# Kernel tuning notes

Hardware: AMD Instinct MI355X
Metric: run time of the kernel (lower is better)

## Reference

```python
import jax, jax.numpy as jnp
import numpy as np

B, NT, NP, C, A = 8, 100, 300, 92, 64
EPS = 1e-7  # keras backend epsilon


def _lsa(cost):
    """Hungarian algorithm (Jonker-Volgenant style), cost [n, m] with n <= m.
    Equivalent to scipy.optimize.linear_sum_assignment."""
    n, m = cost.shape
    if n == 0:
        return np.zeros(0, np.int64), np.zeros(0, np.int64)
    u = np.zeros(n + 1)
    v = np.zeros(m + 1)
    p = np.zeros(m + 1, np.int64)
    way = np.zeros(m + 1, np.int64)
    for i in range(1, n + 1):
        p[0] = i
        j0 = 0
        minv = np.full(m + 1, np.inf)
        used = np.zeros(m + 1, bool)
        while True:
            used[j0] = True
            i0 = p[j0]
            cur = cost[i0 - 1] - u[i0] - v[1:]
            better = (~used[1:]) & (cur < minv[1:])
            minv[1:] = np.where(better, cur, minv[1:])
            way[1:] = np.where(better, j0, way[1:])
            cand = np.where(used[1:], np.inf, minv[1:])
            j1 = int(np.argmin(cand)) + 1
            delta = cand[j1 - 1]
            u[p[used]] += delta
            v[used] -= delta
            minv[~used] -= delta
            j0 = j1
            if p[j0] == 0:
                break
        while j0 != 0:
            j1 = way[j0]
            p[j0] = p[j1]
            j0 = j1
    cols = np.nonzero(p[1:])[0]
    rows = p[1:][cols] - 1
    return rows, cols


def _hungarian_mask(cost, num_objects):
    # mirrors MatchingAssignment.scipy_linear_assignment_mask
    masks = np.zeros(cost.shape, dtype=np.float32)
    for i in range(cost.shape[0]):
        n = int(num_objects[i])
        r, c = _lsa(cost[i, :n, :])
        masks[i][r, c] = 1.0
    return masks


def _focal(y, p):
    # tfa SigmoidFocalCrossEntropy: alpha=0.25, gamma=2.0, probabilities in
    p = jnp.clip(p, EPS, 1.0 - EPS)
    ce = -(y * jnp.log(p) + (1.0 - y) * jnp.log(1.0 - p))
    p_t = y * p + (1.0 - y) * (1.0 - p)
    alpha_f = y * 0.25 + (1.0 - y) * 0.75
    return jnp.sum(alpha_f * (1.0 - p_t) ** 2 * ce, -1)


def _iou_giou(b1, b2):
    # boxes are [ymin, xmin, ymax, xmax] (tfa convention)
    ay1, ax1, ay2, ax2 = b1[..., 0], b1[..., 1], b1[..., 2], b1[..., 3]
    by1, bx1, by2, bx2 = b2[..., 0], b2[..., 1], b2[..., 2], b2[..., 3]
    area_a = jnp.maximum(ay2 - ay1, 0.0) * jnp.maximum(ax2 - ax1, 0.0)
    area_b = jnp.maximum(by2 - by1, 0.0) * jnp.maximum(bx2 - bx1, 0.0)
    inter = (jnp.maximum(jnp.minimum(ay2, by2) - jnp.maximum(ay1, by1), 0.0)
             * jnp.maximum(jnp.minimum(ax2, bx2) - jnp.maximum(ax1, bx1), 0.0))
    union = area_a + area_b - inter
    iou = jnp.where(union > 0, inter / jnp.where(union > 0, union, 1.0), 0.0)
    enc = (jnp.maximum(jnp.maximum(ay2, by2) - jnp.minimum(ay1, by1), 0.0)
           * jnp.maximum(jnp.maximum(ax2, bx2) - jnp.minimum(ax1, bx1), 0.0))
    giou = iou - jnp.where(enc > 0, (enc - union) / jnp.where(enc > 0, enc, 1.0), 0.0)
    return iou, giou


def _cost_arrays(category, attribute, bbox, cat_preds, attribute_preds, box_preds):
    # CostArray: true -> [B,Nt,1,D], pred -> [B,1,Np,D], broadcast -> [B,Nt,Np]
    t_cat = category[:, :, None, :]
    p_cat = cat_preds[:, None, :, :]
    cat_match = jnp.sum((1.0 - p_cat) * t_cat, -1)
    cat_cost = -jnp.sum(jnp.log(p_cat + 1e-5) * t_cat, -1)
    attr_cost = _focal(attribute[:, :, None, :], attribute_preds[:, None, :, :])
    b_t = bbox[:, :, None, :]
    b_p = box_preds[:, None, :, :]
    iou, giou = _iou_giou(b_t, b_p)
    box_cost = 2.0 * (1.0 - giou) + 5.0 * jnp.mean(jnp.abs(b_t - b_p), -1)
    iou_arr = 1.0 - iou  # tfa GIoULoss(mode='iou') returns 1 - iou
    return cat_match, cat_cost, attr_cost, box_cost, iou_arr


def setup_inputs():
    key = jax.random.key(0)
    ks = jax.random.split(key, 9)
    category = jax.nn.one_hot(jax.random.randint(ks[0], (B, NT), 0, C), C, dtype=jnp.float32)
    attribute = (jax.random.uniform(ks[1], (B, NT, A)) < 0.3).astype(jnp.float32)
    yx = jax.random.uniform(ks[2], (B, NT, 2), maxval=0.8)
    hw = jax.random.uniform(ks[3], (B, NT, 2), minval=0.05, maxval=0.2)
    bbox = jnp.concatenate([yx, yx + hw], -1)
    num_objects = jax.random.randint(ks[4], (B,), 1, NT + 1).astype(jnp.int32)
    cat_preds = jax.nn.softmax(jax.random.normal(ks[5], (B, NP, C)), -1)
    attribute_preds = jax.nn.sigmoid(jax.random.normal(ks[6], (B, NP, A)))
    yxp = jax.random.uniform(ks[7], (B, NP, 2), maxval=0.8)
    hwp = jax.random.uniform(ks[8], (B, NP, 2), minval=0.05, maxval=0.2)
    box_preds = jnp.concatenate([yxp, yxp + hwp], -1)
    return dict(category=category, attribute=attribute, bbox=bbox,
                num_objects=num_objects, cat_preds=cat_preds,
                attribute_preds=attribute_preds, box_preds=box_preds)


def reference(category, attribute, bbox, num_objects, cat_preds, attribute_preds, box_preds):
    cat_match, cat_cost_arr, attr_cost_arr, box_cost_arr, iou_arr = _cost_arrays(
        category, attribute, bbox, cat_preds, attribute_preds, box_preds)

    # bipartite matching on CPU (mirrors tf.numpy_function + scipy)
    match_cost = np.asarray(cat_match + box_cost_arr, np.float64)
    mask = jnp.asarray(_hungarian_mask(match_cost, np.asarray(num_objects)))

    total_num_obj = jnp.sum(num_objects).astype(jnp.float32)
    total_num_preds = float(B * NP)

    category_cost = jnp.sum(mask * cat_cost_arr) / total_num_obj
    attribute_cost = jnp.sum(mask * attr_cost_arr) / total_num_obj
    box_cost = jnp.sum(mask * box_cost_arr) / total_num_obj

    # exist loss: keras CategoricalCrossentropy on single-channel probs
    assigned = jnp.max(mask, axis=1)[..., None]  # [B, Np, 1]
    yp = 1.0 - cat_preds[..., 0:1]
    pn = jnp.clip(yp / jnp.sum(yp, -1, keepdims=True), EPS, 1.0 - EPS)
    exist_loss = jnp.sum(-jnp.sum(assigned * jnp.log(pn), -1)) / total_num_preds

    total_loss = category_cost + attribute_cost + box_cost + exist_loss

    masked_iou = mask * iou_arr
    iou_metric = jnp.sum(masked_iou) / total_num_obj
    num_correct_50 = jnp.sum(masked_iou >= 0.5).astype(jnp.float32)
    map_50_95 = jnp.stack([jnp.sum(masked_iou >= r / 100.0).astype(jnp.float32)
                           for r in range(50, 100, 5)]).sum()
    num_predicted = jnp.sum(cat_preds[:, 1, :] < 0.5).astype(jnp.float32)
    mAP50 = num_correct_50 / num_predicted
    map_50_95 = map_50_95 / (num_predicted * 10.0)

    losses = jnp.stack([total_loss, category_cost, attribute_cost, box_cost, exist_loss])
    metrics = jnp.stack([iou_metric, mAP50, map_50_95])
    return losses, metrics
```

## Files before the change

kernel.cpp:

```cpp
#include <hip/hip_runtime.h>
#include <math.h>

#define Bb 8
#define NTt 100
#define NPp 300
#define Cc 92
#define Aa 64


__device__ __forceinline__ void iou_giou_f(const float* bt, const float* bp,
                                           float& iou, float& giou) {
  float ay1 = bt[0], ax1 = bt[1], ay2 = bt[2], ax2 = bt[3];
  float by1 = bp[0], bx1 = bp[1], by2 = bp[2], bx2 = bp[3];
  float area_a = fmaxf(ay2 - ay1, 0.0f) * fmaxf(ax2 - ax1, 0.0f);
  float area_b = fmaxf(by2 - by1, 0.0f) * fmaxf(bx2 - bx1, 0.0f);
  float inter = fmaxf(fminf(ay2, by2) - fmaxf(ay1, by1), 0.0f) *
                fmaxf(fminf(ax2, bx2) - fmaxf(ax1, bx1), 0.0f);
  float un = area_a + area_b - inter;
  iou = (un > 0.0f) ? (inter / un) : 0.0f;
  float enc = fmaxf(fmaxf(ay2, by2) - fminf(ay1, by1), 0.0f) *
              fmaxf(fmaxf(ax2, bx2) - fminf(ax1, bx1), 0.0f);
  giou = iou - ((enc > 0.0f) ? ((enc - un) / enc) : 0.0f);
}

__device__ __forceinline__ float box_cost_f(const float* bt, const float* bp,
                                            float& iou_out) {
  float iou, giou;
  iou_giou_f(bt, bp, iou, giou);
  iou_out = iou;
  float l1 = (fabsf(bt[0] - bp[0]) + fabsf(bt[1] - bp[1]) +
              fabsf(bt[2] - bp[2]) + fabsf(bt[3] - bp[3])) * 0.25f;
  return 2.0f * (1.0f - giou) + 5.0f * l1;
}


template <int CTRL>
__device__ __forceinline__ void dpp_fmin64(double& val) {
  union DU { double d; int i[2]; };
  DU a; a.d = val;
  int lo = __builtin_amdgcn_update_dpp(a.i[0], a.i[0], CTRL, 0xF, 0xF, false);
  int hi = __builtin_amdgcn_update_dpp(a.i[1], a.i[1], CTRL, 0xF, 0xF, false);
  DU o; o.i[0] = lo; o.i[1] = hi;
  val = fmin(val, o.d);
}

__device__ __forceinline__ double wave_fmin64_bcast(double m01) {
  double mvred = m01;
  dpp_fmin64<0x111>(mvred);
  dpp_fmin64<0x112>(mvred);
  dpp_fmin64<0x114>(mvred);
  dpp_fmin64<0x118>(mvred);
  dpp_fmin64<0x142>(mvred);
  dpp_fmin64<0x143>(mvred);
  union DU { double d; int i[2]; };
  DU w; w.d = mvred;
  DU r;
  r.i[0] = __builtin_amdgcn_readlane(w.i[0], 63);
  r.i[1] = __builtin_amdgcn_readlane(w.i[1], 63);
  return r.d;
}

__device__ __forceinline__ double read_u_row(double u_lo, double u_hi, int i0u) {
  int ridx = i0u - 1;
  int src = ridx & 63;
  union DU { double d; int i[2]; };
  DU a, bb, r;
  a.d = u_lo; bb.d = u_hi;
  int lo0 = __builtin_amdgcn_readlane(a.i[0], src);
  int hi0 = __builtin_amdgcn_readlane(a.i[1], src);
  int lo1 = __builtin_amdgcn_readlane(bb.i[0], src);
  int hi1 = __builtin_amdgcn_readlane(bb.i[1], src);
  bool hih = (ridx >> 6) != 0;
  r.i[0] = hih ? lo1 : lo0;
  r.i[1] = hih ? hi1 : hi0;
  return r.d;
}

__device__ __forceinline__ int sel5(int s, int a0, int a1, int a2, int a3, int a4) {
  int r = a4;
  r = (s == 3) ? a3 : r;
  r = (s == 2) ? a2 : r;
  r = (s == 1) ? a1 : r;
  r = (s == 0) ? a0 : r;
  return r;
}


__global__ void __launch_bounds__(64) cost_kernel(
    const float* __restrict__ category, const float* __restrict__ bbox,
    const float* __restrict__ box_preds, const float* __restrict__ cat_preds,
    float* __restrict__ cost, int* __restrict__ cls) {
  int bt = blockIdx.x;
  int b = bt / NTt;
  int lane = threadIdx.x;

  const float* crow = category + (size_t)bt * Cc;
  float c0 = (lane < Cc) ? crow[lane] : 0.0f;
  float c1 = (lane < Cc - 64) ? crow[lane + 64] : 0.0f;
  unsigned long long m0 = __ballot(c0 == 1.0f);
  unsigned long long m1 = __ballot(c1 == 1.0f);
  int cl = m0 ? __builtin_ctzll(m0) : (m1 ? 64 + __builtin_ctzll(m1) : 0);
  if (lane == 0) cls[bt] = cl;

  float tb[4];
  tb[0] = bbox[(size_t)bt * 4 + 0];
  tb[1] = bbox[(size_t)bt * 4 + 1];
  tb[2] = bbox[(size_t)bt * 4 + 2];
  tb[3] = bbox[(size_t)bt * 4 + 3];

  const float4* bp4 = (const float4*)(box_preds + (size_t)b * NPp * 4);
  const float* cp = cat_preds + (size_t)b * NPp * Cc + cl;
  float* crow_out = cost + (size_t)bt * NPp;

  #pragma unroll
  for (int k = 0; k < 5; ++k) {
    int p = lane + (k << 6);
    if (p < NPp) {
      float4 bpv = bp4[p];
      float pb[4] = {bpv.x, bpv.y, bpv.z, bpv.w};
      float iou;
      float bc = box_cost_f(tb, pb, iou);
      float pc = cp[(size_t)p * Cc];
      crow_out[p] = (1.0f - pc) + bc;
    }
  }
}


template <bool STAGE>
__global__ void __launch_bounds__(256, 1) jv_kernel(
    const float* __restrict__ attribute, const float* __restrict__ bbox,
    const int* __restrict__ num_objects, const float* __restrict__ cat_preds,
    const float* __restrict__ attribute_preds, const float* __restrict__ box_preds,
    const float* __restrict__ gcost, const int* __restrict__ gcls,
    double* __restrict__ partials, float* __restrict__ diag) {
  extern __shared__ char smem[];
  const int b = blockIdx.x;
  const int tid = threadIdx.x;
  const int lane = tid & 63;
  const int wid = tid >> 6;

  float* lds_cost = (float*)smem;
  char* tail = smem + (STAGE ? NTt * NPp * 4 : 0);
  int*    cls_l = (int*)tail;
  int*    pj_l  = (int*)(tail + 400);
  double* red   = (double*)(tail + 1616);

  const int n = num_objects[b];
  const float* costg = gcost + (size_t)b * NTt * NPp;

  if (STAGE) {
    const float4* s4 = (const float4*)costg;
    float4* d4 = (float4*)lds_cost;
    int n4 = n * (NPp / 4);
    for (int t = tid; t < n4; t += 256) d4[t] = s4[t];
  }
  for (int t = tid; t < NTt; t += 256) cls_l[t] = gcls[b * NTt + t];
  for (int t = tid; t < 304; t += 256) pj_l[t] = 0;
  __syncthreads();

  const float* costb = STAGE ? lds_cost : costg;

  if (wid == 0) {
    long long t_jv0 = clock64();

    const double INF = __builtin_inf();
    const bool active = lane < 60;
    const int laneOff = active ? 5 * lane : 0;

    double v0 = 0.0, v1 = 0.0, v2 = 0.0, v3 = 0.0, v4 = 0.0;
    double u_lo = 0.0, u_hi = 0.0;
    int wp0 = 0, wp1 = 0, wp2 = 0, wp3 = 0, wp4 = 0;

    float pca = costb[laneOff], pcb = costb[laneOff + 1], pcc = costb[laneOff + 2],
          pcd = costb[laneOff + 3], pce = costb[laneOff + 4];

    for (int i = 1; i <= n; ++i) {
      float ca = pca, cb2 = pcb, cc = pcc, cd = pcd, ce = pce;
      if (i < n) {
        const float* nr = costb + i * NPp + laneOff;
        pca = nr[0]; pcb = nr[1]; pcc = nr[2]; pcd = nr[3]; pce = nr[4];
      }

      double fk0 = (double)ca - v0;
      double fk1 = (double)cb2 - v1;
      double fk2 = (double)cc - v2;
      double fk3 = (double)cd - v3;
      double fk4 = (double)ce - v4;
      double cv0 = active ? fk0 : INF;
      double cv1 = active ? fk1 : INF;
      double cv2 = active ? fk2 : INF;
      double cv3 = active ? fk3 : INF;
      double cv4 = active ? fk4 : INF;

      double m01 = fmin(fmin(fmin(cv0, cv1), fmin(cv2, cv3)), cv4);
      int k0 = (cv3 == m01) ? 3 : 4;
      k0 = (cv2 == m01) ? 2 : k0;
      k0 = (cv1 == m01) ? 1 : k0;
      k0 = (cv0 == m01) ? 0 : k0;
      int ploc = sel5(k0, wp0 & 127, wp1 & 127, wp2 & 127, wp3 & 127, wp4 & 127);
      int p01 = ((laneOff + k0 + 1) << 7) | ploc;

      double delta = wave_fmin64_bcast(m01);
      unsigned long long hit = __ballot(m01 == delta);
      int winlane = __builtin_ctzll(hit);
      int wpk = __builtin_amdgcn_readlane(p01, winlane);
      int j1u = wpk >> 7, i1u = wpk & 127;

      if (i1u == 0) {
        int jm = j1u - 1;
        int wl = jm / 5;
        int sk = jm - 5 * wl;
        if (lane == wl) {
          if      (sk == 0) wp0 = (wp0 & ~127) | i;
          else if (sk == 1) wp1 = (wp1 & ~127) | i;
          else if (sk == 2) wp2 = (wp2 & ~127) | i;
          else if (sk == 3) wp3 = (wp3 & ~127) | i;
          else              wp4 = (wp4 & ~127) | i;
        }
        int ridx = i - 1;
        if ((ridx & 63) == lane) {
          if ((ridx >> 6) == 0) u_lo += delta; else u_hi += delta;
        }
        continue;
      }

      double mv0 = INF, mv1 = INF, mv2 = INF, mv3 = INF, mv4 = INF;
      int usedmask = 0, uf = 0;
      int j0u = 0, i0u = i;

      while (true) {
        { int ridx = i0u - 1; if ((ridx & 63) == lane) uf |= 1 << (ridx >> 6); }

        const float* rowp = costb + (i0u - 1) * NPp + laneOff;
        float fa = rowp[0], fb = rowp[1], fc = rowp[2], fd = rowp[3], fe = rowp[4];
        double ui0 = read_u_row(u_lo, u_hi, i0u);

        {
          double cur = (double)fa - ui0 - v0;
          wp0 = (cur < mv0) ? ((j0u << 7) | (wp0 & 127)) : wp0;
          mv0 = fmin(mv0, cur);
        }
        {
          double cur = (double)fb - ui0 - v1;
          wp1 = (cur < mv1) ? ((j0u << 7) | (wp1 & 127)) : wp1;
          mv1 = fmin(mv1, cur);
        }
        {
          double cur = (double)fc - ui0 - v2;
          wp2 = (cur < mv2) ? ((j0u << 7) | (wp2 & 127)) : wp2;
          mv2 = fmin(mv2, cur);
        }
        {
          double cur = (double)fd - ui0 - v3;
          wp3 = (cur < mv3) ? ((j0u << 7) | (wp3 & 127)) : wp3;
          mv3 = fmin(mv3, cur);
        }
        {
          double cur = (double)fe - ui0 - v4;
          wp4 = (cur < mv4) ? ((j0u << 7) | (wp4 & 127)) : wp4;
          mv4 = fmin(mv4, cur);
        }

        double dv0 = (!active || (usedmask & 1))  ? INF : mv0;
        double dv1 = (!active || (usedmask & 2))  ? INF : mv1;
        double dv2 = (!active || (usedmask & 4))  ? INF : mv2;
        double dv3 = (!active || (usedmask & 8))  ? INF : mv3;
        double dv4 = (!active || (usedmask & 16)) ? INF : mv4;

        double mm = fmin(fmin(fmin(dv0, dv1), fmin(dv2, dv3)), dv4);
        int kk = (dv3 == mm) ? 3 : 4;
        kk = (dv2 == mm) ? 2 : kk;
        kk = (dv1 == mm) ? 1 : kk;
        kk = (dv0 == mm) ? 0 : kk;
        int pl2 = sel5(kk, wp0 & 127, wp1 & 127, wp2 & 127, wp3 & 127, wp4 & 127);
        int pk2 = ((laneOff + kk + 1) << 7) | pl2;

        double delta2 = wave_fmin64_bcast(mm);
        unsigned long long hit2 = __ballot(mm == delta2);
        int winlane2 = __builtin_ctzll(hit2);
        int wpk2 = __builtin_amdgcn_readlane(pk2, winlane2);
        int j1b = wpk2 >> 7, i1b = wpk2 & 127;

        if (uf & 1) u_lo += delta2;
        if (uf & 2) u_hi += delta2;
        v0 -= (usedmask & 1)  ? delta2 : 0.0;
        v1 -= (usedmask & 2)  ? delta2 : 0.0;
        v2 -= (usedmask & 4)  ? delta2 : 0.0;
        v3 -= (usedmask & 8)  ? delta2 : 0.0;
        v4 -= (usedmask & 16) ? delta2 : 0.0;
        mv0 -= delta2; mv1 -= delta2; mv2 -= delta2; mv3 -= delta2; mv4 -= delta2;

        int jm = j1b - 1;
        int wl = jm / 5;
        int sk = jm - 5 * wl;
        if (lane == wl) {
          usedmask |= 1 << sk;
          if      (sk == 0) mv0 = -INF;
          else if (sk == 1) mv1 = -INF;
          else if (sk == 2) mv2 = -INF;
          else if (sk == 3) mv3 = -INF;
          else              mv4 = -INF;
        }

        j0u = j1b; i0u = i1b;
        if (i0u == 0) break;
      }

      {
        int jj = j0u;
        int idx = jj - 1;
        int owner = idx / 5;
        int slot = idx - 5 * owner;
        int f0 = __builtin_amdgcn_readlane(wp0, owner),
            f1 = __builtin_amdgcn_readlane(wp1, owner),
            f2 = __builtin_amdgcn_readlane(wp2, owner),
            f3 = __builtin_amdgcn_readlane(wp3, owner),
            f4 = __builtin_amdgcn_readlane(wp4, owner);
        int wpv = sel5(slot, f0, f1, f2, f3, f4);
        int wayv = wpv >> 7;

        while (true) {
          int jp = wayv;
          int newv;
          int wayn = 0;
          if (jp != 0) {
            int idx2 = jp - 1;
            int owner2 = idx2 / 5;
            int slot2 = idx2 - 5 * owner2;
            int g0 = __builtin_amdgcn_readlane(wp0, owner2),
                g1 = __builtin_amdgcn_readlane(wp1, owner2),
                g2 = __builtin_amdgcn_readlane(wp2, owner2),
                g3 = __builtin_amdgcn_readlane(wp3, owner2),
                g4 = __builtin_amdgcn_readlane(wp4, owner2);
            int wpn = sel5(slot2, g0, g1, g2, g3, g4);
            wayn = wpn >> 7;
            newv = wpn & 127;
          } else {
            newv = i;
          }
          if (lane == owner) {
            if      (slot == 0) wp0 = (wp0 & ~127) | newv;
            else if (slot == 1) wp1 = (wp1 & ~127) | newv;
            else if (slot == 2) wp2 = (wp2 & ~127) | newv;
            else if (slot == 3) wp3 = (wp3 & ~127) | newv;
            else                wp4 = (wp4 & ~127) | newv;
          }
          if (jp == 0) break;
          jj = jp;
          idx = jj - 1;
          owner = idx / 5;
          slot = idx - 5 * owner;
          wayv = wayn;
        }
      }
    }

    long long t_jv1 = clock64();

    if (active) {
      pj_l[5 * lane + 1] = wp0 & 127;
      pj_l[5 * lane + 2] = wp1 & 127;
      pj_l[5 * lane + 3] = wp2 & 127;
      pj_l[5 * lane + 4] = wp3 & 127;
      pj_l[5 * lane + 5] = wp4 & 127;
    }

    if (diag != nullptr && lane == 0) {
      int nl = (int)((t_jv1 - t_jv0) >> 12);
      if (nl > 1024) nl = 1024;
      for (int w2 = 0; w2 < nl; ++w2)
        __builtin_nontemporal_store(1.0f, diag + ((b << 14) + (w2 << 4)));
    }
  }
  __syncthreads();

  double acc[7];
  #pragma unroll
  for (int q = 0; q < 7; ++q) acc[q] = 0.0;

  const float EPSF = 1e-7f;
  const float HIF  = (float)(1.0 - 1e-7);

  for (int j = tid; j < NPp; j += 256) {
    int prowv = pj_l[j + 1];
    if (prowv != 0) {
      int t = prowv - 1;
      int bt = b * NTt + t;
      int idx = b * NPp + j;

      float pc = cat_preds[(size_t)idx * Cc + cls_l[t]];
      acc[0] += (double)(-logf(pc + 1e-5f));

      const float4* yrow4 = (const float4*)(attribute + (size_t)bt * Aa);
      const float4* prw4  = (const float4*)(attribute_preds + (size_t)idx * Aa);
      float af = 0.0f;
      #pragma unroll 4
      for (int a4 = 0; a4 < Aa / 4; ++a4) {
        float4 yv = yrow4[a4];
        float4 pv = prw4[a4];
        float ys[4] = {yv.x, yv.y, yv.z, yv.w};
        float ps[4] = {pv.x, pv.y, pv.z, pv.w};
        #pragma unroll
        for (int e = 0; e < 4; ++e) {
          float y = ys[e];
          float p = fminf(fmaxf(ps[e], EPSF), HIF);
          float cev = -(y * logf(p) + (1.0f - y) * logf(1.0f - p));
          float pt = y * p + (1.0f - y) * (1.0f - p);
          float alpha = y * 0.25f + (1.0f - y) * 0.75f;
          float om = 1.0f - pt;
          af += alpha * (om * om) * cev;
        }
      }
      acc[1] += (double)af;

      const float* btp = bbox + (size_t)bt * 4;
      const float* bpp = box_preds + (size_t)idx * 4;
      float iou;
      float bc = box_cost_f(btp, bpp, iou);
      acc[2] += (double)bc;
      float ia = 1.0f - iou;
      acc[3] += (double)ia;
      if (ia >= 0.5f) acc[5] += 1.0;
      for (int rr = 50; rr < 100; rr += 5) {
        float thr = (float)((double)rr / 100.0);
        if (ia >= thr) acc[6] += 1.0;
      }

      float yp = 1.0f - cat_preds[(size_t)idx * Cc + 0];
      float pn = yp / yp;
      pn = fminf(fmaxf(pn, EPSF), HIF);
      acc[4] += (double)(-logf(pn));
    }
  }

  #pragma unroll
  for (int q = 0; q < 7; ++q) {
    #pragma unroll
    for (int off = 32; off >= 1; off >>= 1) acc[q] += __shfl_xor(acc[q], off);
  }
  if (lane == 0) {
    #pragma unroll
    for (int q = 0; q < 7; ++q) red[wid * 8 + q] = acc[q];
  }

  if (wid == 0) {
    const float* cpb1 = cat_preds + ((size_t)b * NPp + 1) * Cc;
    float q0 = (lane < Cc) ? cpb1[lane] : 1.0f;
    float q1 = (lane + 64 < Cc) ? cpb1[lane + 64] : 1.0f;
    unsigned long long mm0 = __ballot(q0 < 0.5f);
    unsigned long long mm1 = __ballot(q1 < 0.5f);
    if (lane == 0) partials[b * 8 + 7] = (double)(__popcll(mm0) + __popcll(mm1));
  }
  __syncthreads();

  if (tid == 0) {
    #pragma unroll
    for (int q = 0; q < 7; ++q) {
      double s = 0.0;
      for (int w2 = 0; w2 < 4; ++w2) s += red[w2 * 8 + q];
      partials[b * 8 + q] = s;
    }
  }
}


__global__ void combine_kernel(const double* __restrict__ partials,
                               const int* __restrict__ num_objects,
                               float* __restrict__ out) {
  if (threadIdx.x != 0) return;
  double t[8];
  #pragma unroll
  for (int q = 0; q < 8; ++q) t[q] = 0.0;
  for (int b = 0; b < Bb; ++b)
    for (int q = 0; q < 8; ++q) t[q] += partials[b * 8 + q];

  int s = 0;
  for (int b = 0; b < Bb; ++b) s += num_objects[b];
  float tno = (float)s;

  float category_cost  = (float)t[0] / tno;
  float attribute_cost = (float)t[1] / tno;
  float box_cost       = (float)t[2] / tno;
  float exist_loss     = (float)t[4] / (float)(Bb * NPp);
  float total = category_cost + attribute_cost + box_cost + exist_loss;
  float iou_metric = (float)t[3] / tno;
  float npredf = (float)t[7];
  float mAP50 = (float)t[5] / npredf;
  float m5095 = (float)t[6] / (npredf * 10.0f);

  out[0] = total;
  out[1] = category_cost;
  out[2] = attribute_cost;
  out[3] = box_cost;
  out[4] = exist_loss;
  out[5] = iou_metric;
  out[6] = mAP50;
  out[7] = m5095;
}


extern "C" void kernel_launch(void* const* d_in, const int* in_sizes, int n_in,
                              void* d_out, int out_size, void* d_ws, size_t ws_size,
                              hipStream_t stream) {
  const float* category        = (const float*)d_in[0];
  const float* attribute       = (const float*)d_in[1];
  const float* bbox            = (const float*)d_in[2];
  const int*   num_objects     = (const int*)d_in[3];
  const float* cat_preds       = (const float*)d_in[4];
  const float* attribute_preds = (const float*)d_in[5];
  const float* box_preds       = (const float*)d_in[6];
  float* out = (float*)d_out;

  double* partials = (double*)d_ws;
  int*    gcls     = (int*)((char*)d_ws + 512);
  float*  gcost    = (float*)((char*)d_ws + 4096);

  const size_t DIAG_OFF = 970752;
  float* diag = (ws_size >= DIAG_OFF + (size_t)8 * 65536)
                    ? (float*)((char*)d_ws + DIAG_OFF) : nullptr;

  cost_kernel<<<Bb * NTt, 64, 0, stream>>>(category, bbox, box_preds, cat_preds,
                                           gcost, gcls);

  const int STAGED_LDS = NTt * NPp * 4 + 1872;
  const int SMALL_LDS  = 1872;

  hipError_t e = hipFuncSetAttribute(
      reinterpret_cast<const void*>(&jv_kernel<true>),
      hipFuncAttributeMaxDynamicSharedMemorySize, STAGED_LDS);
  if (e == hipSuccess) {
    jv_kernel<true><<<Bb, 256, STAGED_LDS, stream>>>(
        attribute, bbox, num_objects, cat_preds, attribute_preds, box_preds,
        gcost, gcls, partials, diag);
  } else {
    jv_kernel<false><<<Bb, 256, SMALL_LDS, stream>>>(
        attribute, bbox, num_objects, cat_preds, attribute_preds, box_preds,
        gcost, gcls, partials, (float*)nullptr);
  }

  combine_kernel<<<1, 64, 0, stream>>>(partials, num_objects, out);
}
```

Before: 112.6 us.

## Batch JV fast-path rows, drop LDS staging, split loss into parallel kernels

The JV solver now evaluates up to eight rows' unconstrained minima speculatively in a batch. Conflicts are then resolved sequentially, and the full augmenting search runs only for the first row whose best column is already taken. The LDS staging of the cost matrix and the 256-thread block are removed, so the solver runs as a single wave per batch reading global memory. The per-match loss evaluation moves to a separate kernel with one block per prediction, followed by a two-stage reduction. This is meant to shorten the serial critical path and widen the loss work, at the cost of extra launches and of uncached global reads inside the augmenting loop.

```diff
diff --git a/kernel.cpp b/kernel.cpp
--- a/kernel.cpp
+++ b/kernel.cpp
@@ -127,107 +127,90 @@
 }
 
 
-template <bool STAGE>
-__global__ void __launch_bounds__(256, 1) jv_kernel(
-    const float* __restrict__ attribute, const float* __restrict__ bbox,
+__global__ void __launch_bounds__(64, 1) jv_kernel(
     const int* __restrict__ num_objects, const float* __restrict__ cat_preds,
-    const float* __restrict__ attribute_preds, const float* __restrict__ box_preds,
-    const float* __restrict__ gcost, const int* __restrict__ gcls,
+    const float* __restrict__ gcost, int* __restrict__ pj_g,
     double* __restrict__ partials, float* __restrict__ diag) {
-  extern __shared__ char smem[];
   const int b = blockIdx.x;
-  const int tid = threadIdx.x;
-  const int lane = tid & 63;
-  const int wid = tid >> 6;
-
-  float* lds_cost = (float*)smem;
-  char* tail = smem + (STAGE ? NTt * NPp * 4 : 0);
-  int*    cls_l = (int*)tail;
-  int*    pj_l  = (int*)(tail + 400);
-  double* red   = (double*)(tail + 1616);
-
+  const int lane = threadIdx.x;
   const int n = num_objects[b];
-  const float* costg = gcost + (size_t)b * NTt * NPp;
-
-  if (STAGE) {
-    const float4* s4 = (const float4*)costg;
-    float4* d4 = (float4*)lds_cost;
-    int n4 = n * (NPp / 4);
-    for (int t = tid; t < n4; t += 256) d4[t] = s4[t];
-  }
-  for (int t = tid; t < NTt; t += 256) cls_l[t] = gcls[b * NTt + t];
-  for (int t = tid; t < 304; t += 256) pj_l[t] = 0;
-  __syncthreads();
-
-  const float* costb = STAGE ? lds_cost : costg;
-
-  if (wid == 0) {
-    long long t_jv0 = clock64();
-
-    const double INF = __builtin_inf();
-    const bool active = lane < 60;
-    const int laneOff = active ? 5 * lane : 0;
-
-    double v0 = 0.0, v1 = 0.0, v2 = 0.0, v3 = 0.0, v4 = 0.0;
-    double u_lo = 0.0, u_hi = 0.0;
-    int wp0 = 0, wp1 = 0, wp2 = 0, wp3 = 0, wp4 = 0;
-
-    float pca = costb[laneOff], pcb = costb[laneOff + 1], pcc = costb[laneOff + 2],
-          pcd = costb[laneOff + 3], pce = costb[laneOff + 4];
-
-    for (int i = 1; i <= n; ++i) {
-      float ca = pca, cb2 = pcb, cc = pcc, cd = pcd, ce = pce;
-      if (i < n) {
-        const float* nr = costb + i * NPp + laneOff;
-        pca = nr[0]; pcb = nr[1]; pcc = nr[2]; pcd = nr[3]; pce = nr[4];
+  const float* costb = gcost + (size_t)b * NTt * NPp;
+
+  long long t_jv0 = clock64();
+
+  const double INF = __builtin_inf();
+  const bool active = lane < 60;
+  const int laneOff = active ? 5 * lane : 0;
+
+  double v0 = 0.0, v1 = 0.0, v2 = 0.0, v3 = 0.0, v4 = 0.0;
+  double u_lo = 0.0, u_hi = 0.0;
+  int wp0 = 0, wp1 = 0, wp2 = 0, wp3 = 0, wp4 = 0;
+
+  int i = 1;
+  while (i <= n) {
+    int cnt = n - i + 1; if (cnt > 8) cnt = 8;
+    double dly[8]; int jw[8];
+
+    #pragma unroll
+    for (int r = 0; r < 8; ++r) {
+      if (r < cnt) {
+        const float* rowp = costb + (i + r - 1) * NPp + laneOff;
+        float ca = rowp[0], cb2 = rowp[1], cc = rowp[2], cd = rowp[3], ce = rowp[4];
+        double cv0 = active ? (double)ca - v0 : INF;
+        double cv1 = active ? (double)cb2 - v1 : INF;
+        double cv2 = active ? (double)cc - v2 : INF;
+        double cv3 = active ? (double)cd - v3 : INF;
+        double cv4 = active ? (double)ce - v4 : INF;
+        double m01 = fmin(fmin(fmin(cv0, cv1), fmin(cv2, cv3)), cv4);
+        int k0 = (cv3 == m01) ? 3 : 4;
+        k0 = (cv2 == m01) ? 2 : k0;
+        k0 = (cv1 == m01) ? 1 : k0;
+        k0 = (cv0 == m01) ? 0 : k0;
+        int p01 = laneOff + k0 + 1;
+        double delta = wave_fmin64_bcast(m01);
+        unsigned long long hit = __ballot(m01 == delta);
+        int winlane = __builtin_ctzll(hit);
+        dly[r] = delta;
+        jw[r] = __builtin_amdgcn_readlane(p01, winlane);
       }
-
-      double fk0 = (double)ca - v0;
-      double fk1 = (double)cb2 - v1;
-      double fk2 = (double)cc - v2;
-      double fk3 = (double)cd - v3;
-      double fk4 = (double)ce - v4;
-      double cv0 = active ? fk0 : INF;
-      double cv1 = active ? fk1 : INF;
-      double cv2 = active ? fk2 : INF;
-      double cv3 = active ? fk3 : INF;
-      double cv4 = active ? fk4 : INF;
-
-      double m01 = fmin(fmin(fmin(cv0, cv1), fmin(cv2, cv3)), cv4);
-      int k0 = (cv3 == m01) ? 3 : 4;
-      k0 = (cv2 == m01) ? 2 : k0;
-      k0 = (cv1 == m01) ? 1 : k0;
-      k0 = (cv0 == m01) ? 0 : k0;
-      int ploc = sel5(k0, wp0 & 127, wp1 & 127, wp2 & 127, wp3 & 127, wp4 & 127);
-      int p01 = ((laneOff + k0 + 1) << 7) | ploc;
-
-      double delta = wave_fmin64_bcast(m01);
-      unsigned long long hit = __ballot(m01 == delta);
-      int winlane = __builtin_ctzll(hit);
-      int wpk = __builtin_amdgcn_readlane(p01, winlane);
-      int j1u = wpk >> 7, i1u = wpk & 127;
-
-      if (i1u == 0) {
-        int jm = j1u - 1;
-        int wl = jm / 5;
-        int sk = jm - 5 * wl;
-        if (lane == wl) {
-          if      (sk == 0) wp0 = (wp0 & ~127) | i;
-          else if (sk == 1) wp1 = (wp1 & ~127) | i;
-          else if (sk == 2) wp2 = (wp2 & ~127) | i;
-          else if (sk == 3) wp3 = (wp3 & ~127) | i;
-          else              wp4 = (wp4 & ~127) | i;
-        }
-        int ridx = i - 1;
-        if ((ridx & 63) == lane) {
-          if ((ridx >> 6) == 0) u_lo += delta; else u_hi += delta;
-        }
-        continue;
+    }
+
+    int consumed = 0, fbrow = 0;
+    #pragma unroll
+    for (int r = 0; r < 8; ++r) {
+      if (r < cnt && fbrow == 0) {
+        int row = i + r;
+        int j1 = jw[r];
+        int jm = j1 - 1, ow = jm / 5, sk = jm - 5 * ow;
+        int o0 = __builtin_amdgcn_readlane(wp0, ow);
+        int o1 = __builtin_amdgcn_readlane(wp1, ow);
+        int o2 = __builtin_amdgcn_readlane(wp2, ow);
+        int o3 = __builtin_amdgcn_readlane(wp3, ow);
+        int o4 = __builtin_amdgcn_readlane(wp4, ow);
+        int occ = sel5(sk, o0 & 127, o1 & 127, o2 & 127, o3 & 127, o4 & 127);
+        consumed = r + 1;
+        if (occ == 0) {
+          if (lane == ow) {
+            if      (sk == 0) wp0 = (wp0 & ~127) | row;
+            else if (sk == 1) wp1 = (wp1 & ~127) | row;
+            else if (sk == 2) wp2 = (wp2 & ~127) | row;
+            else if (sk == 3) wp3 = (wp3 & ~127) | row;
+            else              wp4 = (wp4 & ~127) | row;
+          }
+          int ridx = row - 1;
+          if ((ridx & 63) == lane) {
+            if (ridx >> 6) u_hi += dly[r]; else u_lo += dly[r];
+          }
+        } else {
+          fbrow = row;
+        }
       }
-
+    }
+
+    if (fbrow) {
       double mv0 = INF, mv1 = INF, mv2 = INF, mv3 = INF, mv4 = INF;
       int usedmask = 0, uf = 0;
-      int j0u = 0, i0u = i;
+      int j0u = 0, i0u = fbrow;
 
       while (true) {
         { int ridx = i0u - 1; if ((ridx & 63) == lane) uf |= 1 << (ridx >> 6); }
@@ -337,7 +320,7 @@
             wayn = wpn >> 7;
             newv = wpn & 127;
           } else {
-            newv = i;
+            newv = fbrow;
           }
           if (lane == owner) {
             if      (slot == 0) wp0 = (wp0 & ~127) | newv;
@@ -356,118 +339,126 @@
       }
     }
 
-    long long t_jv1 = clock64();
-
-    if (active) {
-      pj_l[5 * lane + 1] = wp0 & 127;
-      pj_l[5 * lane + 2] = wp1 & 127;
-      pj_l[5 * lane + 3] = wp2 & 127;
-      pj_l[5 * lane + 4] = wp3 & 127;
-      pj_l[5 * lane + 5] = wp4 & 127;
-    }
-
-    if (diag != nullptr && lane == 0) {
-      int nl = (int)((t_jv1 - t_jv0) >> 12);
-      if (nl > 1024) nl = 1024;
-      for (int w2 = 0; w2 < nl; ++w2)
-        __builtin_nontemporal_store(1.0f, diag + ((b << 14) + (w2 << 4)));
-    }
-  }
-  __syncthreads();
-
-  double acc[7];
-  #pragma unroll
-  for (int q = 0; q < 7; ++q) acc[q] = 0.0;
+    i += consumed;
+  }
+
+  long long t_jv1 = clock64();
+
+  if (active) {
+    int base = b * 304;
+    pj_g[base + 5 * lane + 1] = wp0 & 127;
+    pj_g[base + 5 * lane + 2] = wp1 & 127;
+    pj_g[base + 5 * lane + 3] = wp2 & 127;
+    pj_g[base + 5 * lane + 4] = wp3 & 127;
+    pj_g[base + 5 * lane + 5] = wp4 & 127;
+  }
+
+  const float* cpb1 = cat_preds + ((size_t)b * NPp + 1) * Cc;
+  float q0 = (lane < Cc) ? cpb1[lane] : 1.0f;
+  float q1 = (lane + 64 < Cc) ? cpb1[lane + 64] : 1.0f;
+  unsigned long long mm0 = __ballot(q0 < 0.5f);
+  unsigned long long mm1 = __ballot(q1 < 0.5f);
+  if (lane == 0) partials[b * 8 + 7] = (double)(__popcll(mm0) + __popcll(mm1));
+
+  if (diag != nullptr && lane == 0) {
+    int nl = (int)((t_jv1 - t_jv0) >> 12);
+    if (nl > 256) nl = 256;
+    for (int w2 = 0; w2 < nl; ++w2)
+      __builtin_nontemporal_store(1.0f, diag + ((b << 12) + (w2 << 4)));
+  }
+}
+
+
+__global__ void __launch_bounds__(64) loss_kernel(
+    const float* __restrict__ attribute, const float* __restrict__ bbox,
+    const float* __restrict__ cat_preds, const float* __restrict__ attribute_preds,
+    const float* __restrict__ box_preds, const int* __restrict__ gcls,
+    const int* __restrict__ pj_g, double* __restrict__ colpart) {
+  int gb = blockIdx.x;
+  int b = gb / NPp;
+  int j = gb - b * NPp;
+  int lane = threadIdx.x;
+  double* outp = colpart + (size_t)gb * 8;
+
+  int prow = pj_g[b * 304 + j + 1];
+  if (prow == 0) {
+    if (lane < 8) outp[lane] = 0.0;
+    return;
+  }
+
+  int t = prow - 1;
+  int bt = b * NTt + t;
 
   const float EPSF = 1e-7f;
   const float HIF  = (float)(1.0 - 1e-7);
 
-  for (int j = tid; j < NPp; j += 256) {
-    int prowv = pj_l[j + 1];
-    if (prowv != 0) {
-      int t = prowv - 1;
-      int bt = b * NTt + t;
-      int idx = b * NPp + j;
-
-      float pc = cat_preds[(size_t)idx * Cc + cls_l[t]];
-      acc[0] += (double)(-logf(pc + 1e-5f));
-
-      const float4* yrow4 = (const float4*)(attribute + (size_t)bt * Aa);
-      const float4* prw4  = (const float4*)(attribute_preds + (size_t)idx * Aa);
-      float af = 0.0f;
-      #pragma unroll 4
-      for (int a4 = 0; a4 < Aa / 4; ++a4) {
-        float4 yv = yrow4[a4];
-        float4 pv = prw4[a4];
-        float ys[4] = {yv.x, yv.y, yv.z, yv.w};
-        float ps[4] = {pv.x, pv.y, pv.z, pv.w};
-        #pragma unroll
-        for (int e = 0; e < 4; ++e) {
-          float y = ys[e];
-          float p = fminf(fmaxf(ps[e], EPSF), HIF);
-          float cev = -(y * logf(p) + (1.0f - y) * logf(1.0f - p));
-          float pt = y * p + (1.0f - y) * (1.0f - p);
-          float alpha = y * 0.25f + (1.0f - y) * 0.75f;
-          float om = 1.0f - pt;
-          af += alpha * (om * om) * cev;
-        }
-      }
-      acc[1] += (double)af;
-
-      const float* btp = bbox + (size_t)bt * 4;
-      const float* bpp = box_preds + (size_t)idx * 4;
-      float iou;
-      float bc = box_cost_f(btp, bpp, iou);
-      acc[2] += (double)bc;
-      float ia = 1.0f - iou;
-      acc[3] += (double)ia;
-      if (ia >= 0.5f) acc[5] += 1.0;
-      for (int rr = 50; rr < 100; rr += 5) {
-        float thr = (float)((double)rr / 100.0);
-        if (ia >= thr) acc[6] += 1.0;
-      }
-
-      float yp = 1.0f - cat_preds[(size_t)idx * Cc + 0];
-      float pn = yp / yp;
-      pn = fminf(fmaxf(pn, EPSF), HIF);
-      acc[4] += (double)(-logf(pn));
+  float y = attribute[(size_t)bt * Aa + lane];
+  float p = fminf(fmaxf(attribute_preds[(size_t)gb * Aa + lane], EPSF), HIF);
+  float ce = -(y * logf(p) + (1.0f - y) * logf(1.0f - p));
+  float pt = y * p + (1.0f - y) * (1.0f - p);
+  float alpha = y * 0.25f + (1.0f - y) * 0.75f;
+  float om = 1.0f - pt;
+  double sattr = (double)(alpha * (om * om) * ce);
+  #pragma unroll
+  for (int off = 32; off >= 1; off >>= 1) sattr += __shfl_xor(sattr, off);
+
+  if (lane == 0) {
+    int cl = gcls[bt];
+    float pc = cat_preds[(size_t)gb * Cc + cl];
+    double scat = (double)(-logf(pc + 1e-5f));
+
+    const float* btp = bbox + (size_t)bt * 4;
+    const float* bpp = box_preds + (size_t)gb * 4;
+    float iou;
+    float bc = box_cost_f(btp, bpp, iou);
+    float ia = 1.0f - iou;
+
+    double c50 = (ia >= 0.5f) ? 1.0 : 0.0;
+    double call = 0.0;
+    for (int rr = 50; rr < 100; rr += 5) {
+      float thr = (float)((double)rr / 100.0);
+      if (ia >= thr) call += 1.0;
     }
-  }
-
+
+    float yp = 1.0f - cat_preds[(size_t)gb * Cc + 0];
+    float pn = yp / yp;
+    pn = fminf(fmaxf(pn, EPSF), HIF);
+    double sex = (double)(-logf(pn));
+
+    outp[0] = scat;
+    outp[1] = sattr;
+    outp[2] = (double)bc;
+    outp[3] = (double)ia;
+    outp[4] = sex;
+    outp[5] = c50;
+    outp[6] = call;
+    outp[7] = 0.0;
+  }
+}
+
+
+__global__ void __launch_bounds__(64) combine1_kernel(
+    const double* __restrict__ colpart, double* __restrict__ partials) {
+  int bid = blockIdx.x;
+  int b = bid / 7;
+  int q = bid - b * 7;
+  int lane = threadIdx.x;
+
+  double s = 0.0;
   #pragma unroll
-  for (int q = 0; q < 7; ++q) {
-    #pragma unroll
-    for (int off = 32; off >= 1; off >>= 1) acc[q] += __shfl_xor(acc[q], off);
-  }
-  if (lane == 0) {
-    #pragma unroll
-    for (int q = 0; q < 7; ++q) red[wid * 8 + q] = acc[q];
-  }
-
-  if (wid == 0) {
-    const float* cpb1 = cat_preds + ((size_t)b * NPp + 1) * Cc;
-    float q0 = (lane < Cc) ? cpb1[lane] : 1.0f;
-    float q1 = (lane + 64 < Cc) ? cpb1[lane + 64] : 1.0f;
-    unsigned long long mm0 = __ballot(q0 < 0.5f);
-    unsigned long long mm1 = __ballot(q1 < 0.5f);
-    if (lane == 0) partials[b * 8 + 7] = (double)(__popcll(mm0) + __popcll(mm1));
-  }
-  __syncthreads();
-
-  if (tid == 0) {
-    #pragma unroll
-    for (int q = 0; q < 7; ++q) {
-      double s = 0.0;
-      for (int w2 = 0; w2 < 4; ++w2) s += red[w2 * 8 + q];
-      partials[b * 8 + q] = s;
-    }
-  }
-}
-
-
-__global__ void combine_kernel(const double* __restrict__ partials,
-                               const int* __restrict__ num_objects,
-                               float* __restrict__ out) {
+  for (int k = 0; k < 5; ++k) {
+    int j = lane + (k << 6);
+    if (j < NPp) s += colpart[((size_t)(b * NPp + j)) * 8 + q];
+  }
+  #pragma unroll
+  for (int off = 32; off >= 1; off >>= 1) s += __shfl_xor(s, off);
+  if (lane == 0) partials[b * 8 + q] = s;
+}
+
+
+__global__ void final_kernel(const double* __restrict__ partials,
+                             const int* __restrict__ num_objects,
+                             float* __restrict__ out) {
   if (threadIdx.x != 0) return;
   double t[8];
   #pragma unroll
@@ -515,29 +506,20 @@
   double* partials = (double*)d_ws;
   int*    gcls     = (int*)((char*)d_ws + 512);
   float*  gcost    = (float*)((char*)d_ws + 4096);
-
-  const size_t DIAG_OFF = 970752;
-  float* diag = (ws_size >= DIAG_OFF + (size_t)8 * 65536)
+  int*    pj_g     = (int*)((char*)d_ws + 964096);
+  double* colpart  = (double*)((char*)d_ws + 973824);
+
+  const size_t DIAG_OFF = 1127424;
+  float* diag = (ws_size >= DIAG_OFF + (size_t)8 * 16384)
                     ? (float*)((char*)d_ws + DIAG_OFF) : nullptr;
 
   cost_kernel<<<Bb * NTt, 64, 0, stream>>>(category, bbox, box_preds, cat_preds,
                                            gcost, gcls);
-
-  const int STAGED_LDS = NTt * NPp * 4 + 1872;
-  const int SMALL_LDS  = 1872;
-
-  hipError_t e = hipFuncSetAttribute(
-      reinterpret_cast<const void*>(&jv_kernel<true>),
-      hipFuncAttributeMaxDynamicSharedMemorySize, STAGED_LDS);
-  if (e == hipSuccess) {
-    jv_kernel<true><<<Bb, 256, STAGED_LDS, stream>>>(
-        attribute, bbox, num_objects, cat_preds, attribute_preds, box_preds,
-        gcost, gcls, partials, diag);
-  } else {
-    jv_kernel<false><<<Bb, 256, SMALL_LDS, stream>>>(
-        attribute, bbox, num_objects, cat_preds, attribute_preds, box_preds,
-        gcost, gcls, partials, (float*)nullptr);
-  }
-
-  combine_kernel<<<1, 64, 0, stream>>>(partials, num_objects, out);
-}
+  jv_kernel<<<Bb, 64, 0, stream>>>(num_objects, cat_preds, gcost, pj_g,
+                                   partials, diag);
+  loss_kernel<<<Bb * NPp, 64, 0, stream>>>(attribute, bbox, cat_preds,
+                                           attribute_preds, box_preds, gcls,
+                                           pj_g, colpart);
+  combine1_kernel<<<Bb * 7, 64, 0, stream>>>(colpart, partials);
+  final_kernel<<<1, 64, 0, stream>>>(partials, num_objects, out);
+}
```

After: 140.5 us. 1.25x slower.
